# Kernel tuning notes

Hardware: AMD Instinct MI355X
Metric: run time of the kernel (lower is better)

## Reference

```python
import jax, jax.numpy as jnp
import numpy as np

N = 100000   # nodes
E = 1600000  # edges
G = 512      # graphs
IN_F = 128
HID = 64
EPS = 1e-5


def setup_inputs() -> dict:
    key = jax.random.key(0)
    ks = jax.random.split(key, 16)
    x = jax.random.normal(ks[0], (N, IN_F), dtype=jnp.float32)
    edge_index = jax.random.randint(ks[1], (2, E), 0, N, dtype=jnp.int64)
    batch = jnp.sort(jax.random.randint(ks[2], (N,), 0, G, dtype=jnp.int64))
    s = 0.05
    return {
        'x': x, 'edge_index': edge_index, 'batch': batch,
        'W1': jax.random.normal(ks[3], (IN_F, HID), jnp.float32) * s,
        'b1': jax.random.normal(ks[4], (HID,), jnp.float32) * s,
        'g1': jax.random.uniform(ks[5], (HID,), jnp.float32),
        'be1': jax.random.normal(ks[6], (HID,), jnp.float32) * s,
        'rm1': jnp.zeros((HID,), jnp.float32),
        'rv1': jnp.ones((HID,), jnp.float32),
        'W2': jax.random.normal(ks[7], (HID, HID), jnp.float32) * s,
        'b2': jax.random.normal(ks[8], (HID,), jnp.float32) * s,
        'g2': jax.random.uniform(ks[9], (HID,), jnp.float32),
        'be2': jax.random.normal(ks[10], (HID,), jnp.float32) * s,
        'rm2': jnp.zeros((HID,), jnp.float32),
        'rv2': jnp.ones((HID,), jnp.float32),
        'Wh1': jax.random.normal(ks[11], (2 * HID, HID), jnp.float32) * s,
        'bh1': jax.random.normal(ks[12], (HID,), jnp.float32) * s,
        'Wh2': jax.random.normal(ks[13], (HID, HID // 2), jnp.float32) * s,
        'bh2': jnp.zeros((HID // 2,), jnp.float32),
        'Wh3': jax.random.normal(ks[14], (HID // 2, 1), jnp.float32) * s,
        'bh3': jnp.zeros((1,), jnp.float32),
    }


def _gcn(h, W, b, src, dst):
    # GCNConv with added self-loops and symmetric D^{-1/2} A D^{-1/2} normalization
    hw = h @ W                                   # [N, HID]
    deg = jnp.ones((N,), hw.dtype).at[dst].add(1.0)  # in-degree + self-loop
    dinv = jax.lax.rsqrt(deg)
    norm = dinv[src] * dinv[dst]                 # [E]
    agg = jax.ops.segment_sum(hw[src] * norm[:, None], dst, num_segments=N)
    return agg + hw * (dinv * dinv)[:, None] + b  # self-loop term + bias


def _bn(x, g, b, rm, rv):
    return (x - rm) * jax.lax.rsqrt(rv + EPS) * g + b


def reference(x, edge_index, batch, W1, b1, g1, be1, rm1, rv1,
              W2, b2, g2, be2, rm2, rv2, Wh1, bh1, Wh2, bh2, Wh3, bh3):
    src, dst = edge_index[0], edge_index[1]
    # layer 0 (no residual: dim change 128 -> 64)
    h = jax.nn.relu(_bn(_gcn(x, W1, b1, src, dst), g1, be1, rm1, rv1))
    # layer 1 with residual
    h = h + jax.nn.relu(_bn(_gcn(h, W2, b2, src, dst), g2, be2, rm2, rv2))
    # global mean + max pooling per graph
    ones = jnp.ones((N,), h.dtype)
    cnt = jnp.maximum(jax.ops.segment_sum(ones, batch, num_segments=G), 1.0)
    h_mean = jax.ops.segment_sum(h, batch, num_segments=G) / cnt[:, None]
    h_max = jax.ops.segment_max(h, batch, num_segments=G)
    hg = jnp.concatenate([h_mean, h_max], axis=-1)   # [G, 2*HID]
    # MLP head (dropout disabled in eval)
    z = jax.nn.relu(hg @ Wh1 + bh1)
    z = jax.nn.relu(z @ Wh2 + bh2)
    out = z @ Wh3 + bh3
    return jax.nn.sigmoid(out).squeeze(-1)           # [G]
```

## Files before the change

### kernel.cpp

```cpp
#include <hip/hip_runtime.h>
#include <math.h>

#define NN 100000
#define EE 1600000
#define GG 512
#define INF_ 128
#define HID 64
#define EPS 1e-5f

#define NBUK 391
#define P1_TILES 98
#define P1_PAD 104
#define GB_B 25
#define GEMM1_B 1563

typedef unsigned int uint32;
typedef __attribute__((ext_vector_type(8))) short bf16x8;
typedef __attribute__((ext_vector_type(4))) float f32x4;
typedef __attribute__((ext_vector_type(2))) float f32x2;

static __device__ inline uint32 f2bf(float f) {
    uint32 u = __float_as_uint(f);
    return (u + 0x7FFFu + ((u >> 16) & 1u)) >> 16;
}


template <int K, bool SCALE>
__device__ __forceinline__ void gemm_body(const float* __restrict__ X,
        const float* __restrict__ W, const float* __restrict__ dinv,
        uint32* __restrict__ outb, int nrows, int bx,
        unsigned short* __restrict__ Al, unsigned short* __restrict__ Bl) {
    constexpr int KP = K + 8;
    int tid = threadIdx.x;
    for (int i = tid; i < 64 * (K / 2); i += 256) {
        int n = i & 63, kp = i >> 6;
        uint32 lo = f2bf(W[(size_t)(2 * kp) * 64 + n]);
        uint32 hi = f2bf(W[(size_t)(2 * kp + 1) * 64 + n]);
        *(uint32*)&Bl[n * KP + kp * 2] = lo | (hi << 16);
    }
    int r0 = bx * 64;
    const float* Xb = X + (size_t)r0 * K;
    int limit = (nrows - r0) * K;
    for (int f = tid * 4; f < 64 * K; f += 1024) {
        float4 v = {0.f, 0.f, 0.f, 0.f};
        if (f + 3 < limit) v = *(const float4*)&Xb[f];
        int row = f / K, kpos = f % K;
        ushort4 pk;
        pk.x = (unsigned short)f2bf(v.x);
        pk.y = (unsigned short)f2bf(v.y);
        pk.z = (unsigned short)f2bf(v.z);
        pk.w = (unsigned short)f2bf(v.w);
        *(ushort4*)&Al[row * KP + kpos] = pk;
    }
    __syncthreads();
    int lane = tid & 63, wv = tid >> 6;
    int m = lane & 15, quad = lane >> 4;
    f32x4 acc0 = {0.f, 0.f, 0.f, 0.f}, acc1 = acc0, acc2 = acc0, acc3 = acc0;
    int arow = wv * 16 + m;
#pragma unroll
    for (int k0 = 0; k0 < K; k0 += 32) {
        int koff = k0 + quad * 8;
        bf16x8 a = *(const bf16x8*)&Al[arow * KP + koff];
        bf16x8 b0 = *(const bf16x8*)&Bl[(0 * 16 + m) * KP + koff];
        bf16x8 b1 = *(const bf16x8*)&Bl[(1 * 16 + m) * KP + koff];
        bf16x8 b2 = *(const bf16x8*)&Bl[(2 * 16 + m) * KP + koff];
        bf16x8 b3 = *(const bf16x8*)&Bl[(3 * 16 + m) * KP + koff];
        acc0 = __builtin_amdgcn_mfma_f32_16x16x32_bf16(a, b0, acc0, 0, 0, 0);
        acc1 = __builtin_amdgcn_mfma_f32_16x16x32_bf16(a, b1, acc1, 0, 0, 0);
        acc2 = __builtin_amdgcn_mfma_f32_16x16x32_bf16(a, b2, acc2, 0, 0, 0);
        acc3 = __builtin_amdgcn_mfma_f32_16x16x32_bf16(a, b3, acc3, 0, 0, 0);
    }
    float dv[4];
#pragma unroll
    for (int reg = 0; reg < 4; ++reg) {
        int row = r0 + wv * 16 + quad * 4 + reg;
        if (SCALE) dv[reg] = (row < nrows) ? dinv[row] : 0.f;
        else       dv[reg] = 1.f;
    }
    const float* accs[4] = {(const float*)&acc0, (const float*)&acc1,
                            (const float*)&acc2, (const float*)&acc3};
#pragma unroll
    for (int nt = 0; nt < 4; ++nt) {
#pragma unroll
        for (int reg = 0; reg < 4; ++reg) {
            float val = accs[nt][reg] * dv[reg];
            float v1 = __shfl_down(val, 1);
            float v2 = __shfl_down(val, 2);
            float v3 = __shfl_down(val, 3);
            int row = r0 + wv * 16 + quad * 4 + reg;
            if (((m & 3) == 0) && row < nrows) {
                int u = __builtin_amdgcn_cvt_pk_fp8_f32(val, v1, 0, false);
                u = __builtin_amdgcn_cvt_pk_fp8_f32(v2, v3, u, true);
                outb[(size_t)row * 16 + nt * 4 + (m >> 2)] = (uint32)u;
            }
        }
    }
}

__global__ __launch_bounds__(256) void k_mega(const int* __restrict__ ei,
        int* __restrict__ hblk, const int* __restrict__ bat, int* __restrict__ gb,
        const float* __restrict__ x, const float* __restrict__ W1,
        uint32* __restrict__ hwb,
        const float* b1, const float* g1, const float* be1,
        const float* rm1, const float* rv1,
        const float* b2, const float* g2, const float* be2,
        const float* rm2, const float* rv2, float* sc) {
    __shared__ alignas(16) char smem[64 * (INF_ + 8) * 2 * 2];
    int b = blockIdx.x, t = threadIdx.x;
    if (b < P1_TILES) {
        int* h = (int*)smem;
        for (int i = t; i < NBUK; i += 256) h[i] = 0;
        __syncthreads();
        const int4* dst4 = (const int4*)(ei + EE);
        int base4 = b * 4096;
        for (int j = 0; j < 16; ++j) {
            int i4 = base4 + j * 256 + t;
            if (i4 < EE / 4) {
                int4 d = dst4[i4];
                atomicAdd(&h[d.x >> 8], 1);
                atomicAdd(&h[d.y >> 8], 1);
                atomicAdd(&h[d.z >> 8], 1);
                atomicAdd(&h[d.w >> 8], 1);
            }
        }
        __syncthreads();
        for (int i = t; i < NBUK; i += 256) hblk[i * P1_PAD + b] = h[i];
    } else if (b < P1_TILES + GB_B) {
        int gid = (b - P1_TILES) * 256 + t;
        for (int i = gid; i < NN; i += GB_B * 256) {
            int bi = bat[i];
            if (i == 0) {
                for (int g = 0; g <= bi; ++g) gb[g] = 0;
            } else {
                int bp = bat[i - 1];
                for (int g = bp + 1; g <= bi; ++g) gb[g] = i;
            }
            if (i == NN - 1)
                for (int g = bi + 1; g <= GG; ++g) gb[g] = NN;
        }
    } else if (b < P1_TILES + GB_B + 1) {
        if (t < 64) {
            int l = t;
            float s1 = g1[l] * rsqrtf(rv1[l] + EPS);
            sc[l]       = s1;
            sc[64 + l]  = (b1[l] - rm1[l]) * s1 + be1[l];
            float s2 = g2[l] * rsqrtf(rv2[l] + EPS);
            sc[128 + l] = s2;
            sc[192 + l] = (b2[l] - rm2[l]) * s2 + be2[l];
        } else if (t < 80) {
            hwb[(size_t)NN * 16 + (t - 64)] = 0u;
        }
        for (int i = t; i < NBUK * (P1_PAD - P1_TILES); i += 256) {
            int k = i / (P1_PAD - P1_TILES);
            int bb = P1_TILES + i % (P1_PAD - P1_TILES);
            hblk[k * P1_PAD + bb] = 0;
        }
    } else {
        int bx = b - P1_TILES - GB_B - 1;
        unsigned short* Al = (unsigned short*)smem;
        unsigned short* Bl = (unsigned short*)(smem + 64 * (INF_ + 8) * 2);
        gemm_body<INF_, false>(x, W1, nullptr, hwb, NN, bx, Al, Bl);
    }
}

__global__ __launch_bounds__(512) void k_p1b(const int* __restrict__ ei,
                                             const int* __restrict__ hblk,
                                             uint32* __restrict__ pairs,
                                             int* __restrict__ bbase,
                                             int* __restrict__ offs) {
    __shared__ int h[NBUK];
    __shared__ int wsum[8];
    int b = blockIdx.x, t = threadIdx.x;
    int part = 0, c = 0;
    if (t < NBUK) {
        const int4* row = (const int4*)(hblk + t * P1_PAD);
#pragma unroll
        for (int q = 0; q < P1_PAD / 4; ++q) {
            int4 v = row[q];
            c += v.x + v.y + v.z + v.w;
            part += ((4 * q + 0 < b) ? v.x : 0) + ((4 * q + 1 < b) ? v.y : 0)
                  + ((4 * q + 2 < b) ? v.z : 0) + ((4 * q + 3 < b) ? v.w : 0);
        }
    }
    int lane = t & 63, w = t >> 6;
    int v = c;
    for (int d = 1; d < 64; d <<= 1) { int n = __shfl_up(v, d); if (lane >= d) v += n; }
    if (lane == 63) wsum[w] = v;
    __syncthreads();
    int pre = 0;
    for (int q = 0; q < w; ++q) pre += wsum[q];
    int excl = pre + v - c;
    if (t < NBUK) h[t] = excl + part;
    if (b == 0) {
        if (t <= NBUK) bbase[t] = excl;
        if (t == 0) offs[NN] = EE;
    }
    __syncthreads();
    const int4* src4 = (const int4*)ei;
    const int4* dst4 = (const int4*)(ei + EE);
    int base4 = b * 4096;
    for (int j = 0; j < 8; ++j) {
        int i4 = base4 + j * 512 + t;
        if (i4 < EE / 4) {
            int4 d = dst4[i4];
            int4 s = src4[i4];
            int p0 = atomicAdd(&h[d.x >> 8], 1);
            pairs[p0] = ((uint32)s.x << 8) | (uint32)(d.x & 255);
            int p1 = atomicAdd(&h[d.y >> 8], 1);
            pairs[p1] = ((uint32)s.y << 8) | (uint32)(d.y & 255);
            int p2 = atomicAdd(&h[d.z >> 8], 1);
            pairs[p2] = ((uint32)s.z << 8) | (uint32)(d.z & 255);
            int p3 = atomicAdd(&h[d.w >> 8], 1);
            pairs[p3] = ((uint32)s.w << 8) | (uint32)(d.w & 255);
        }
    }
}

__global__ __launch_bounds__(256) void k_p2(const uint32* __restrict__ pairs,
                                            const int* __restrict__ bbase,
                                            int* __restrict__ offs, float* __restrict__ dinv,
                                            int* __restrict__ col) {
    int b = blockIdx.x, t = threadIdx.x;
    int nbase = b << 8;
    int ebase = bbase[b], eend = bbase[b + 1];
    int m = eend - ebase;
    __shared__ int cnt[256];
    __shared__ int wsum[4];
    cnt[t] = 0;
    __syncthreads();
    for (int i = t; i < m; i += 256)
        atomicAdd(&cnt[pairs[ebase + i] & 255u], 1);
    __syncthreads();
    int c = cnt[t];
    int lane = t & 63, w = t >> 6;
    int v = c;
    for (int d = 1; d < 64; d <<= 1) { int n = __shfl_up(v, d); if (lane >= d) v += n; }
    if (lane == 63) wsum[w] = v;
    __syncthreads();
    int pre = 0;
    for (int q = 0; q < w; ++q) pre += wsum[q];
    int excl = pre + v - c;
    int node = nbase + t;
    if (node < NN) {
        offs[node] = ebase + excl;
        dinv[node] = rsqrtf(1.f + (float)c);
    }
    __syncthreads();
    cnt[t] = excl;
    __syncthreads();
    for (int i = t; i < m; i += 256) {
        uint32 u = pairs[ebase + i];
        int loc = atomicAdd(&cnt[u & 255u], 1);
        col[ebase + loc] = (int)(u >> 8);
    }
}

__global__ void k_gcn_gather_w(const uint32* __restrict__ hwb, const int* __restrict__ col,
                               const int* __restrict__ offs,
                               const float* __restrict__ dinv, const float* __restrict__ scale,
                               const float* __restrict__ shift,
                               float* __restrict__ out) {
    int node = blockIdx.x * 4 + (threadIdx.x >> 6);
    if (node >= NN) return;
    int lane = threadIdx.x & 63;
    int quarter = lane >> 4;
    int fl = lane & 15;
    int e0 = offs[node], e1 = offs[node + 1];
    float di = dinv[node];
    uint32 uself = hwb[(size_t)node * 16 + fl];
    float a0 = 0.f, a1 = 0.f, a2 = 0.f, a3 = 0.f;
    float b0 = 0.f, b1 = 0.f, b2 = 0.f, b3 = 0.f;
    for (int base = e0; base < e1; base += 64) {
        int m = e1 - base; if (m > 64) m = 64;
        int srcv = NN; float wv = 0.f;
        if (lane < m) { srcv = col[base + lane]; wv = dinv[srcv]; }
        for (int j = 0; j < m; j += 16) {
            int   s0 = __shfl(srcv, j + quarter);
            int   s1 = __shfl(srcv, j + 4 + quarter);
            int   s2 = __shfl(srcv, j + 8 + quarter);
            int   s3 = __shfl(srcv, j + 12 + quarter);
            float w0 = __shfl(wv, j + quarter);
            float w1 = __shfl(wv, j + 4 + quarter);
            float w2 = __shfl(wv, j + 8 + quarter);
            float w3 = __shfl(wv, j + 12 + quarter);
            uint32 u0 = hwb[(size_t)s0 * 16 + fl];
            uint32 u1 = hwb[(size_t)s1 * 16 + fl];
            uint32 u2 = hwb[(size_t)s2 * 16 + fl];
            uint32 u3 = hwb[(size_t)s3 * 16 + fl];
            f32x2 l0 = __builtin_amdgcn_cvt_pk_f32_fp8((int)u0, false);
            f32x2 h0 = __builtin_amdgcn_cvt_pk_f32_fp8((int)u0, true);
            f32x2 l1 = __builtin_amdgcn_cvt_pk_f32_fp8((int)u1, false);
            f32x2 h1 = __builtin_amdgcn_cvt_pk_f32_fp8((int)u1, true);
            f32x2 l2 = __builtin_amdgcn_cvt_pk_f32_fp8((int)u2, false);
            f32x2 h2 = __builtin_amdgcn_cvt_pk_f32_fp8((int)u2, true);
            f32x2 l3 = __builtin_amdgcn_cvt_pk_f32_fp8((int)u3, false);
            f32x2 h3 = __builtin_amdgcn_cvt_pk_f32_fp8((int)u3, true);
            a0 = fmaf(l0[0], w0, a0); a1 = fmaf(l0[1], w0, a1);
            a2 = fmaf(h0[0], w0, a2); a3 = fmaf(h0[1], w0, a3);
            b0 = fmaf(l1[0], w1, b0); b1 = fmaf(l1[1], w1, b1);
            b2 = fmaf(h1[0], w1, b2); b3 = fmaf(h1[1], w1, b3);
            a0 = fmaf(l2[0], w2, a0); a1 = fmaf(l2[1], w2, a1);
            a2 = fmaf(h2[0], w2, a2); a3 = fmaf(h2[1], w2, a3);
            b0 = fmaf(l3[0], w3, b0); b1 = fmaf(l3[1], w3, b1);
            b2 = fmaf(h3[0], w3, b2); b3 = fmaf(h3[1], w3, b3);
        }
    }
    a0 += b0; a1 += b1; a2 += b2; a3 += b3;
    a0 += __shfl_xor(a0, 16); a0 += __shfl_xor(a0, 32);
    a1 += __shfl_xor(a1, 16); a1 += __shfl_xor(a1, 32);
    a2 += __shfl_xor(a2, 16); a2 += __shfl_xor(a2, 32);
    a3 += __shfl_xor(a3, 16); a3 += __shfl_xor(a3, 32);
    if (quarter == 0) {
        f32x2 slo = __builtin_amdgcn_cvt_pk_f32_fp8((int)uself, false);
        f32x2 shi = __builtin_amdgcn_cvt_pk_f32_fp8((int)uself, true);
        float dii = di * di;
        float4 sc4 = *(const float4*)&scale[4 * fl];
        float4 sh4 = *(const float4*)&shift[4 * fl];
        float v0 = fmaf(a0 * di + slo[0] * dii, sc4.x, sh4.x);
        float v1 = fmaf(a1 * di + slo[1] * dii, sc4.y, sh4.y);
        float v2 = fmaf(a2 * di + shi[0] * dii, sc4.z, sh4.z);
        float v3 = fmaf(a3 * di + shi[1] * dii, sc4.w, sh4.w);
        float4 o;
        o.x = fmaxf(v0, 0.f); o.y = fmaxf(v1, 0.f);
        o.z = fmaxf(v2, 0.f); o.w = fmaxf(v3, 0.f);
        *(float4*)&out[(size_t)node * 64 + 4 * fl] = o;
    }
}

__global__ void k_gcn_gather(const uint32* __restrict__ hwb, const int* __restrict__ col,
                             const int* __restrict__ offs,
                             const float* __restrict__ dinv, const float* __restrict__ scale,
                             const float* __restrict__ shift, const float* __restrict__ resid,
                             float* __restrict__ out) {
    int node = blockIdx.x * 4 + (threadIdx.x >> 6);
    if (node >= NN) return;
    int lane = threadIdx.x & 63;
    int quarter = lane >> 4;
    int fl = lane & 15;
    int e0 = offs[node], e1 = offs[node + 1];
    float di = dinv[node];
    uint32 uself = hwb[(size_t)node * 16 + fl];
    float a0 = 0.f, a1 = 0.f, a2 = 0.f, a3 = 0.f;
    float b0 = 0.f, b1 = 0.f, b2 = 0.f, b3 = 0.f;
    for (int base = e0; base < e1; base += 64) {
        int m = e1 - base; if (m > 64) m = 64;
        int srcv = NN;
        if (lane < m) srcv = col[base + lane];
        for (int j = 0; j < m; j += 16) {
            int s0 = __shfl(srcv, j + quarter);
            int s1 = __shfl(srcv, j + 4 + quarter);
            int s2 = __shfl(srcv, j + 8 + quarter);
            int s3 = __shfl(srcv, j + 12 + quarter);
            uint32 u0 = hwb[(size_t)s0 * 16 + fl];
            uint32 u1 = hwb[(size_t)s1 * 16 + fl];
            uint32 u2 = hwb[(size_t)s2 * 16 + fl];
            uint32 u3 = hwb[(size_t)s3 * 16 + fl];
            f32x2 l0 = __builtin_amdgcn_cvt_pk_f32_fp8((int)u0, false);
            f32x2 h0 = __builtin_amdgcn_cvt_pk_f32_fp8((int)u0, true);
            f32x2 l1 = __builtin_amdgcn_cvt_pk_f32_fp8((int)u1, false);
            f32x2 h1 = __builtin_amdgcn_cvt_pk_f32_fp8((int)u1, true);
            f32x2 l2 = __builtin_amdgcn_cvt_pk_f32_fp8((int)u2, false);
            f32x2 h2 = __builtin_amdgcn_cvt_pk_f32_fp8((int)u2, true);
            f32x2 l3 = __builtin_amdgcn_cvt_pk_f32_fp8((int)u3, false);
            f32x2 h3 = __builtin_amdgcn_cvt_pk_f32_fp8((int)u3, true);
            a0 += l0[0]; a1 += l0[1]; a2 += h0[0]; a3 += h0[1];
            b0 += l1[0]; b1 += l1[1]; b2 += h1[0]; b3 += h1[1];
            a0 += l2[0]; a1 += l2[1]; a2 += h2[0]; a3 += h2[1];
            b0 += l3[0]; b1 += l3[1]; b2 += h3[0]; b3 += h3[1];
        }
    }
    a0 += b0; a1 += b1; a2 += b2; a3 += b3;
    a0 += __shfl_xor(a0, 16); a0 += __shfl_xor(a0, 32);
    a1 += __shfl_xor(a1, 16); a1 += __shfl_xor(a1, 32);
    a2 += __shfl_xor(a2, 16); a2 += __shfl_xor(a2, 32);
    a3 += __shfl_xor(a3, 16); a3 += __shfl_xor(a3, 32);
    if (quarter == 0) {
        f32x2 slo = __builtin_amdgcn_cvt_pk_f32_fp8((int)uself, false);
        f32x2 shi = __builtin_amdgcn_cvt_pk_f32_fp8((int)uself, true);
        float4 sc4 = *(const float4*)&scale[4 * fl];
        float4 sh4 = *(const float4*)&shift[4 * fl];
        float v0 = fmaf((a0 + slo[0]) * di, sc4.x, sh4.x);
        float v1 = fmaf((a1 + slo[1]) * di, sc4.y, sh4.y);
        float v2 = fmaf((a2 + shi[0]) * di, sc4.z, sh4.z);
        float v3 = fmaf((a3 + shi[1]) * di, sc4.w, sh4.w);
        float4 rv = *(const float4*)&resid[(size_t)node * 64 + 4 * fl];
        float4 o;
        o.x = fmaxf(v0, 0.f) + rv.x;
        o.y = fmaxf(v1, 0.f) + rv.y;
        o.z = fmaxf(v2, 0.f) + rv.z;
        o.w = fmaxf(v3, 0.f) + rv.w;
        *(float4*)&out[(size_t)node * 64 + 4 * fl] = o;
    }
}

__global__ void k_poolhead(const float* __restrict__ h, const int* __restrict__ gb,
                           const float* __restrict__ Wh1, const float* __restrict__ bh1,
                           const float* __restrict__ Wh2, const float* __restrict__ bh2,
                           const float* __restrict__ Wh3, const float* __restrict__ bh3,
                           float* __restrict__ out) {
    int g = blockIdx.x, t = threadIdx.x;
    int lo = gb[g], hi = gb[g + 1];
    float s0 = 0.f, s1 = 0.f, s2 = 0.f, s3 = 0.f;
    float s4 = 0.f, s5 = 0.f, s6 = 0.f, s7 = 0.f;
    float m0 = 0.f, m1 = 0.f, m2 = 0.f, m3 = 0.f;
    float m4 = 0.f, m5 = 0.f, m6 = 0.f, m7 = 0.f;
    int i = lo;
    for (; i + 8 <= hi; i += 8) {
        float v0 = h[(size_t)(i + 0) * 64 + t];
        float v1 = h[(size_t)(i + 1) * 64 + t];
        float v2 = h[(size_t)(i + 2) * 64 + t];
        float v3 = h[(size_t)(i + 3) * 64 + t];
        float v4 = h[(size_t)(i + 4) * 64 + t];
        float v5 = h[(size_t)(i + 5) * 64 + t];
        float v6 = h[(size_t)(i + 6) * 64 + t];
        float v7 = h[(size_t)(i + 7) * 64 + t];
        s0 += v0; m0 = fmaxf(m0, v0);
        s1 += v1; m1 = fmaxf(m1, v1);
        s2 += v2; m2 = fmaxf(m2, v2);
        s3 += v3; m3 = fmaxf(m3, v3);
        s4 += v4; m4 = fmaxf(m4, v4);
        s5 += v5; m5 = fmaxf(m5, v5);
        s6 += v6; m6 = fmaxf(m6, v6);
        s7 += v7; m7 = fmaxf(m7, v7);
    }
    for (; i < hi; ++i) {
        float v = h[(size_t)i * 64 + t];
        s0 += v; m0 = fmaxf(m0, v);
    }
    float sum = ((s0 + s1) + (s2 + s3)) + ((s4 + s5) + (s6 + s7));
    float mx = fmaxf(fmaxf(fmaxf(m0, m1), fmaxf(m2, m3)),
                     fmaxf(fmaxf(m4, m5), fmaxf(m6, m7)));
    float c = fmaxf((float)(hi - lo), 1.f);
    __shared__ float hg[128];
    __shared__ float z1[64];
    __shared__ float z2[32];
    hg[t]      = sum / c;
    hg[64 + t] = mx;
    __syncthreads();
    float acc = bh1[t];
#pragma unroll 8
    for (int k = 0; k < 128; ++k) acc = fmaf(hg[k], Wh1[k * 64 + t], acc);
    z1[t] = fmaxf(acc, 0.f);
    __syncthreads();
    if (t < 32) {
        float a2 = bh2[t];
#pragma unroll 8
        for (int k = 0; k < 64; ++k) a2 = fmaf(z1[k], Wh2[k * 32 + t], a2);
        z2[t] = fmaxf(a2, 0.f);
    }
    __syncthreads();
    if (t == 0) {
        float a3 = bh3[0];
        for (int k = 0; k < 32; ++k) a3 = fmaf(z2[k], Wh3[k], a3);
        out[g] = 1.f / (1.f + expf(-a3));
    }
}

__global__ __launch_bounds__(256) void k_gemm2(const float* __restrict__ X,
                                               const float* __restrict__ W,
                                               const float* __restrict__ dinv,
                                               uint32* __restrict__ outb) {
    __shared__ alignas(16) unsigned short Al[64 * (HID + 8)];
    __shared__ alignas(16) unsigned short Bl[64 * (HID + 8)];
    gemm_body<HID, true>(X, W, dinv, outb, NN, blockIdx.x, Al, Bl);
}


static inline size_t alignup(size_t x) { return (x + 255) & ~(size_t)255; }

extern "C" void kernel_launch(void* const* d_in, const int* in_sizes, int n_in,
                              void* d_out, int out_size, void* d_ws, size_t ws_size,
                              hipStream_t stream) {
    const float* x   = (const float*)d_in[0];
    const int*   ei  = (const int*)d_in[1];
    const int*   bat = (const int*)d_in[2];
    const float* W1  = (const float*)d_in[3];
    const float* b1  = (const float*)d_in[4];
    const float* g1  = (const float*)d_in[5];
    const float* be1 = (const float*)d_in[6];
    const float* rm1 = (const float*)d_in[7];
    const float* rv1 = (const float*)d_in[8];
    const float* W2  = (const float*)d_in[9];
    const float* b2  = (const float*)d_in[10];
    const float* g2  = (const float*)d_in[11];
    const float* be2 = (const float*)d_in[12];
    const float* rm2 = (const float*)d_in[13];
    const float* rv2 = (const float*)d_in[14];
    const float* Wh1 = (const float*)d_in[15];
    const float* bh1 = (const float*)d_in[16];
    const float* Wh2 = (const float*)d_in[17];
    const float* bh2 = (const float*)d_in[18];
    const float* Wh3 = (const float*)d_in[19];
    const float* bh3 = (const float*)d_in[20];
    float* out = (float*)d_out;

    char* ws = (char*)d_ws;
    size_t o = 0;
    int*   hblk   = (int*)(ws + o);  o = alignup(o + (size_t)NBUK * P1_PAD * 4);
    int*   bbase  = (int*)(ws + o);  o = alignup(o + (NBUK + 1) * 4);
    int*   offs   = (int*)(ws + o);  o = alignup(o + (NN + 1) * 4);
    uint32* pairs = (uint32*)(ws + o); o = alignup(o + (size_t)EE * 4);
    int*   col    = (int*)(ws + o);  o = alignup(o + (size_t)EE * 4);
    float* dinv   = (float*)(ws + o); o = alignup(o + (size_t)NN * 4);
    float* scb    = (float*)(ws + o); o = alignup(o + 4 * 64 * 4);
    int*   gb     = (int*)(ws + o);  o = alignup(o + (GG + 1) * 4);
    uint32* hwb   = (uint32*)(ws + o); o = alignup(o + (size_t)(NN + 1) * 16 * 4);
    float* h      = (float*)(ws + o); o = alignup(o + (size_t)NN * 64 * 4);
    (void)ws_size; (void)n_in; (void)in_sizes; (void)out_size;

    k_mega<<<P1_TILES + GB_B + 1 + GEMM1_B, 256, 0, stream>>>(
        ei, hblk, bat, gb, x, W1, hwb,
        b1, g1, be1, rm1, rv1, b2, g2, be2, rm2, rv2, scb);
    k_p1b<<<P1_TILES, 512, 0, stream>>>(ei, hblk, pairs, bbase, offs);
    k_p2<<<NBUK, 256, 0, stream>>>(pairs, bbase, offs, dinv, col);

    k_gcn_gather_w<<<(NN + 3) / 4, 256, 0, stream>>>(hwb, col, offs, dinv,
                                                     scb, scb + 64, h);
    k_gemm2<<<GEMM1_B, 256, 0, stream>>>(h, W2, dinv, hwb);
    k_gcn_gather<<<(NN + 3) / 4, 256, 0, stream>>>(hwb, col, offs, dinv,
                                                   scb + 128, scb + 192, h, h);
    k_poolhead<<<GG, 64, 0, stream>>>(h, gb, Wh1, bh1, Wh2, bh2, Wh3, bh3, out);
}
```

Before: 284.8 us.

## Store layer-1 activations as bf16 and process two nodes per wave in gathers

Result: faster. 270.9 us (median of 2 runs) (-4.9%).

```diff
diff --git a/kernel.cpp b/kernel.cpp
--- a/kernel.cpp
+++ b/kernel.cpp
@@ -23,6 +23,8 @@
     uint32 u = __float_as_uint(f);
     return (u + 0x7FFFu + ((u >> 16) & 1u)) >> 16;
 }
+static __device__ inline float bf_lo(uint32 u) { return __uint_as_float(u << 16); }
+static __device__ inline float bf_hi(uint32 u) { return __uint_as_float(u & 0xFFFF0000u); }
 
 
 template <int K, bool SCALE>
@@ -259,137 +261,247 @@
                                const int* __restrict__ offs,
                                const float* __restrict__ dinv, const float* __restrict__ scale,
                                const float* __restrict__ shift,
-                               float* __restrict__ out) {
-    int node = blockIdx.x * 4 + (threadIdx.x >> 6);
-    if (node >= NN) return;
+                               uint32* __restrict__ out) {
+    int nodeA = blockIdx.x * 8 + (threadIdx.x >> 6) * 2;
+    if (nodeA >= NN) return;
+    int nodeB = nodeA + 1;
+    int hasB = nodeB < NN;
     int lane = threadIdx.x & 63;
     int quarter = lane >> 4;
     int fl = lane & 15;
-    int e0 = offs[node], e1 = offs[node + 1];
-    float di = dinv[node];
-    uint32 uself = hwb[(size_t)node * 16 + fl];
-    float a0 = 0.f, a1 = 0.f, a2 = 0.f, a3 = 0.f;
-    float b0 = 0.f, b1 = 0.f, b2 = 0.f, b3 = 0.f;
-    for (int base = e0; base < e1; base += 64) {
-        int m = e1 - base; if (m > 64) m = 64;
-        int srcv = NN; float wv = 0.f;
-        if (lane < m) { srcv = col[base + lane]; wv = dinv[srcv]; }
-        for (int j = 0; j < m; j += 16) {
-            int   s0 = __shfl(srcv, j + quarter);
-            int   s1 = __shfl(srcv, j + 4 + quarter);
-            int   s2 = __shfl(srcv, j + 8 + quarter);
-            int   s3 = __shfl(srcv, j + 12 + quarter);
-            float w0 = __shfl(wv, j + quarter);
-            float w1 = __shfl(wv, j + 4 + quarter);
-            float w2 = __shfl(wv, j + 8 + quarter);
-            float w3 = __shfl(wv, j + 12 + quarter);
-            uint32 u0 = hwb[(size_t)s0 * 16 + fl];
-            uint32 u1 = hwb[(size_t)s1 * 16 + fl];
-            uint32 u2 = hwb[(size_t)s2 * 16 + fl];
-            uint32 u3 = hwb[(size_t)s3 * 16 + fl];
-            f32x2 l0 = __builtin_amdgcn_cvt_pk_f32_fp8((int)u0, false);
-            f32x2 h0 = __builtin_amdgcn_cvt_pk_f32_fp8((int)u0, true);
-            f32x2 l1 = __builtin_amdgcn_cvt_pk_f32_fp8((int)u1, false);
-            f32x2 h1 = __builtin_amdgcn_cvt_pk_f32_fp8((int)u1, true);
-            f32x2 l2 = __builtin_amdgcn_cvt_pk_f32_fp8((int)u2, false);
-            f32x2 h2 = __builtin_amdgcn_cvt_pk_f32_fp8((int)u2, true);
-            f32x2 l3 = __builtin_amdgcn_cvt_pk_f32_fp8((int)u3, false);
-            f32x2 h3 = __builtin_amdgcn_cvt_pk_f32_fp8((int)u3, true);
-            a0 = fmaf(l0[0], w0, a0); a1 = fmaf(l0[1], w0, a1);
-            a2 = fmaf(h0[0], w0, a2); a3 = fmaf(h0[1], w0, a3);
-            b0 = fmaf(l1[0], w1, b0); b1 = fmaf(l1[1], w1, b1);
-            b2 = fmaf(h1[0], w1, b2); b3 = fmaf(h1[1], w1, b3);
-            a0 = fmaf(l2[0], w2, a0); a1 = fmaf(l2[1], w2, a1);
-            a2 = fmaf(h2[0], w2, a2); a3 = fmaf(h2[1], w2, a3);
-            b0 = fmaf(l3[0], w3, b0); b1 = fmaf(l3[1], w3, b1);
-            b2 = fmaf(h3[0], w3, b2); b3 = fmaf(h3[1], w3, b3);
-        }
-    }
-    a0 += b0; a1 += b1; a2 += b2; a3 += b3;
-    a0 += __shfl_xor(a0, 16); a0 += __shfl_xor(a0, 32);
-    a1 += __shfl_xor(a1, 16); a1 += __shfl_xor(a1, 32);
-    a2 += __shfl_xor(a2, 16); a2 += __shfl_xor(a2, 32);
-    a3 += __shfl_xor(a3, 16); a3 += __shfl_xor(a3, 32);
+    int eA0 = offs[nodeA], eA1 = offs[nodeA + 1];
+    int eB1 = hasB ? offs[nodeB + 1] : eA1;
+    int eB0 = eA1;
+    float diA = dinv[nodeA];
+    float diB = hasB ? dinv[nodeB] : 0.f;
+    uint32 uselfA = hwb[(size_t)nodeA * 16 + fl];
+    uint32 uselfB = hwb[(size_t)(hasB ? nodeB : NN) * 16 + fl];
+    float aA0 = 0.f, aA1 = 0.f, aA2 = 0.f, aA3 = 0.f;
+    float aB0 = 0.f, aB1 = 0.f, aB2 = 0.f, aB3 = 0.f;
+    int baseA = eA0, baseB = eB0;
+    while (baseA < eA1 || baseB < eB1) {
+        int mA = eA1 - baseA; mA = mA < 0 ? 0 : (mA > 64 ? 64 : mA);
+        int mB = eB1 - baseB; mB = mB < 0 ? 0 : (mB > 64 ? 64 : mB);
+        int sA = NN; float wA = 0.f;
+        if (lane < mA) { sA = col[baseA + lane]; wA = dinv[sA]; }
+        int sB = NN; float wB = 0.f;
+        if (lane < mB) { sB = col[baseB + lane]; wB = dinv[sB]; }
+        int mm = mA > mB ? mA : mB;
+        for (int j = 0; j < mm; j += 16) {
+            int   sa0 = __shfl(sA, j + quarter);
+            int   sa1 = __shfl(sA, j + 4 + quarter);
+            int   sa2 = __shfl(sA, j + 8 + quarter);
+            int   sa3 = __shfl(sA, j + 12 + quarter);
+            int   sb0 = __shfl(sB, j + quarter);
+            int   sb1 = __shfl(sB, j + 4 + quarter);
+            int   sb2 = __shfl(sB, j + 8 + quarter);
+            int   sb3 = __shfl(sB, j + 12 + quarter);
+            float wa0 = __shfl(wA, j + quarter);
+            float wa1 = __shfl(wA, j + 4 + quarter);
+            float wa2 = __shfl(wA, j + 8 + quarter);
+            float wa3 = __shfl(wA, j + 12 + quarter);
+            float wb0 = __shfl(wB, j + quarter);
+            float wb1 = __shfl(wB, j + 4 + quarter);
+            float wb2 = __shfl(wB, j + 8 + quarter);
+            float wb3 = __shfl(wB, j + 12 + quarter);
+            uint32 ua0 = hwb[(size_t)sa0 * 16 + fl];
+            uint32 ua1 = hwb[(size_t)sa1 * 16 + fl];
+            uint32 ua2 = hwb[(size_t)sa2 * 16 + fl];
+            uint32 ua3 = hwb[(size_t)sa3 * 16 + fl];
+            uint32 ub0 = hwb[(size_t)sb0 * 16 + fl];
+            uint32 ub1 = hwb[(size_t)sb1 * 16 + fl];
+            uint32 ub2 = hwb[(size_t)sb2 * 16 + fl];
+            uint32 ub3 = hwb[(size_t)sb3 * 16 + fl];
+            f32x2 la0 = __builtin_amdgcn_cvt_pk_f32_fp8((int)ua0, false);
+            f32x2 ha0 = __builtin_amdgcn_cvt_pk_f32_fp8((int)ua0, true);
+            f32x2 la1 = __builtin_amdgcn_cvt_pk_f32_fp8((int)ua1, false);
+            f32x2 ha1 = __builtin_amdgcn_cvt_pk_f32_fp8((int)ua1, true);
+            f32x2 la2 = __builtin_amdgcn_cvt_pk_f32_fp8((int)ua2, false);
+            f32x2 ha2 = __builtin_amdgcn_cvt_pk_f32_fp8((int)ua2, true);
+            f32x2 la3 = __builtin_amdgcn_cvt_pk_f32_fp8((int)ua3, false);
+            f32x2 ha3 = __builtin_amdgcn_cvt_pk_f32_fp8((int)ua3, true);
+            f32x2 lb0 = __builtin_amdgcn_cvt_pk_f32_fp8((int)ub0, false);
+            f32x2 hb0 = __builtin_amdgcn_cvt_pk_f32_fp8((int)ub0, true);
+            f32x2 lb1 = __builtin_amdgcn_cvt_pk_f32_fp8((int)ub1, false);
+            f32x2 hb1 = __builtin_amdgcn_cvt_pk_f32_fp8((int)ub1, true);
+            f32x2 lb2 = __builtin_amdgcn_cvt_pk_f32_fp8((int)ub2, false);
+            f32x2 hb2 = __builtin_amdgcn_cvt_pk_f32_fp8((int)ub2, true);
+            f32x2 lb3 = __builtin_amdgcn_cvt_pk_f32_fp8((int)ub3, false);
+            f32x2 hb3 = __builtin_amdgcn_cvt_pk_f32_fp8((int)ub3, true);
+            aA0 = fmaf(la0[0], wa0, aA0); aA1 = fmaf(la0[1], wa0, aA1);
+            aA2 = fmaf(ha0[0], wa0, aA2); aA3 = fmaf(ha0[1], wa0, aA3);
+            aB0 = fmaf(lb0[0], wb0, aB0); aB1 = fmaf(lb0[1], wb0, aB1);
+            aB2 = fmaf(hb0[0], wb0, aB2); aB3 = fmaf(hb0[1], wb0, aB3);
+            aA0 = fmaf(la1[0], wa1, aA0); aA1 = fmaf(la1[1], wa1, aA1);
+            aA2 = fmaf(ha1[0], wa1, aA2); aA3 = fmaf(ha1[1], wa1, aA3);
+            aB0 = fmaf(lb1[0], wb1, aB0); aB1 = fmaf(lb1[1], wb1, aB1);
+            aB2 = fmaf(hb1[0], wb1, aB2); aB3 = fmaf(hb1[1], wb1, aB3);
+            aA0 = fmaf(la2[0], wa2, aA0); aA1 = fmaf(la2[1], wa2, aA1);
+            aA2 = fmaf(ha2[0], wa2, aA2); aA3 = fmaf(ha2[1], wa2, aA3);
+            aB0 = fmaf(lb2[0], wb2, aB0); aB1 = fmaf(lb2[1], wb2, aB1);
+            aB2 = fmaf(hb2[0], wb2, aB2); aB3 = fmaf(hb2[1], wb2, aB3);
+            aA0 = fmaf(la3[0], wa3, aA0); aA1 = fmaf(la3[1], wa3, aA1);
+            aA2 = fmaf(ha3[0], wa3, aA2); aA3 = fmaf(ha3[1], wa3, aA3);
+            aB0 = fmaf(lb3[0], wb3, aB0); aB1 = fmaf(lb3[1], wb3, aB1);
+            aB2 = fmaf(hb3[0], wb3, aB2); aB3 = fmaf(hb3[1], wb3, aB3);
+        }
+        baseA += 64; baseB += 64;
+    }
+    aA0 += __shfl_xor(aA0, 16); aA0 += __shfl_xor(aA0, 32);
+    aA1 += __shfl_xor(aA1, 16); aA1 += __shfl_xor(aA1, 32);
+    aA2 += __shfl_xor(aA2, 16); aA2 += __shfl_xor(aA2, 32);
+    aA3 += __shfl_xor(aA3, 16); aA3 += __shfl_xor(aA3, 32);
+    aB0 += __shfl_xor(aB0, 16); aB0 += __shfl_xor(aB0, 32);
+    aB1 += __shfl_xor(aB1, 16); aB1 += __shfl_xor(aB1, 32);
+    aB2 += __shfl_xor(aB2, 16); aB2 += __shfl_xor(aB2, 32);
+    aB3 += __shfl_xor(aB3, 16); aB3 += __shfl_xor(aB3, 32);
     if (quarter == 0) {
-        f32x2 slo = __builtin_amdgcn_cvt_pk_f32_fp8((int)uself, false);
-        f32x2 shi = __builtin_amdgcn_cvt_pk_f32_fp8((int)uself, true);
-        float dii = di * di;
         float4 sc4 = *(const float4*)&scale[4 * fl];
         float4 sh4 = *(const float4*)&shift[4 * fl];
-        float v0 = fmaf(a0 * di + slo[0] * dii, sc4.x, sh4.x);
-        float v1 = fmaf(a1 * di + slo[1] * dii, sc4.y, sh4.y);
-        float v2 = fmaf(a2 * di + shi[0] * dii, sc4.z, sh4.z);
-        float v3 = fmaf(a3 * di + shi[1] * dii, sc4.w, sh4.w);
-        float4 o;
-        o.x = fmaxf(v0, 0.f); o.y = fmaxf(v1, 0.f);
-        o.z = fmaxf(v2, 0.f); o.w = fmaxf(v3, 0.f);
-        *(float4*)&out[(size_t)node * 64 + 4 * fl] = o;
+        f32x2 sloA = __builtin_amdgcn_cvt_pk_f32_fp8((int)uselfA, false);
+        f32x2 shiA = __builtin_amdgcn_cvt_pk_f32_fp8((int)uselfA, true);
+        float diiA = diA * diA;
+        float v0 = fmaf(aA0 * diA + sloA[0] * diiA, sc4.x, sh4.x);
+        float v1 = fmaf(aA1 * diA + sloA[1] * diiA, sc4.y, sh4.y);
+        float v2 = fmaf(aA2 * diA + shiA[0] * diiA, sc4.z, sh4.z);
+        float v3 = fmaf(aA3 * diA + shiA[1] * diiA, sc4.w, sh4.w);
+        v0 = fmaxf(v0, 0.f); v1 = fmaxf(v1, 0.f);
+        v2 = fmaxf(v2, 0.f); v3 = fmaxf(v3, 0.f);
+        uint2 oA;
+        oA.x = f2bf(v0) | (f2bf(v1) << 16);
+        oA.y = f2bf(v2) | (f2bf(v3) << 16);
+        *(uint2*)&out[(size_t)nodeA * 32 + 2 * fl] = oA;
+        if (hasB) {
+            f32x2 sloB = __builtin_amdgcn_cvt_pk_f32_fp8((int)uselfB, false);
+            f32x2 shiB = __builtin_amdgcn_cvt_pk_f32_fp8((int)uselfB, true);
+            float diiB = diB * diB;
+            float w0 = fmaf(aB0 * diB + sloB[0] * diiB, sc4.x, sh4.x);
+            float w1 = fmaf(aB1 * diB + sloB[1] * diiB, sc4.y, sh4.y);
+            float w2 = fmaf(aB2 * diB + shiB[0] * diiB, sc4.z, sh4.z);
+            float w3 = fmaf(aB3 * diB + shiB[1] * diiB, sc4.w, sh4.w);
+            w0 = fmaxf(w0, 0.f); w1 = fmaxf(w1, 0.f);
+            w2 = fmaxf(w2, 0.f); w3 = fmaxf(w3, 0.f);
+            uint2 oB;
+            oB.x = f2bf(w0) | (f2bf(w1) << 16);
+            oB.y = f2bf(w2) | (f2bf(w3) << 16);
+            *(uint2*)&out[(size_t)nodeB * 32 + 2 * fl] = oB;
+        }
     }
 }
 
 __global__ void k_gcn_gather(const uint32* __restrict__ hwb, const int* __restrict__ col,
                              const int* __restrict__ offs,
                              const float* __restrict__ dinv, const float* __restrict__ scale,
-                             const float* __restrict__ shift, const float* __restrict__ resid,
+                             const float* __restrict__ shift, const uint32* __restrict__ resid,
                              float* __restrict__ out) {
-    int node = blockIdx.x * 4 + (threadIdx.x >> 6);
-    if (node >= NN) return;
+    int nodeA = blockIdx.x * 8 + (threadIdx.x >> 6) * 2;
+    if (nodeA >= NN) return;
+    int nodeB = nodeA + 1;
+    int hasB = nodeB < NN;
     int lane = threadIdx.x & 63;
     int quarter = lane >> 4;
     int fl = lane & 15;
-    int e0 = offs[node], e1 = offs[node + 1];
-    float di = dinv[node];
-    uint32 uself = hwb[(size_t)node * 16 + fl];
-    float a0 = 0.f, a1 = 0.f, a2 = 0.f, a3 = 0.f;
-    float b0 = 0.f, b1 = 0.f, b2 = 0.f, b3 = 0.f;
-    for (int base = e0; base < e1; base += 64) {
-        int m = e1 - base; if (m > 64) m = 64;
-        int srcv = NN;
-        if (lane < m) srcv = col[base + lane];
-        for (int j = 0; j < m; j += 16) {
-            int s0 = __shfl(srcv, j + quarter);
-            int s1 = __shfl(srcv, j + 4 + quarter);
-            int s2 = __shfl(srcv, j + 8 + quarter);
-            int s3 = __shfl(srcv, j + 12 + quarter);
-            uint32 u0 = hwb[(size_t)s0 * 16 + fl];
-            uint32 u1 = hwb[(size_t)s1 * 16 + fl];
-            uint32 u2 = hwb[(size_t)s2 * 16 + fl];
-            uint32 u3 = hwb[(size_t)s3 * 16 + fl];
-            f32x2 l0 = __builtin_amdgcn_cvt_pk_f32_fp8((int)u0, false);
-            f32x2 h0 = __builtin_amdgcn_cvt_pk_f32_fp8((int)u0, true);
-            f32x2 l1 = __builtin_amdgcn_cvt_pk_f32_fp8((int)u1, false);
-            f32x2 h1 = __builtin_amdgcn_cvt_pk_f32_fp8((int)u1, true);
-            f32x2 l2 = __builtin_amdgcn_cvt_pk_f32_fp8((int)u2, false);
-            f32x2 h2 = __builtin_amdgcn_cvt_pk_f32_fp8((int)u2, true);
-            f32x2 l3 = __builtin_amdgcn_cvt_pk_f32_fp8((int)u3, false);
-            f32x2 h3 = __builtin_amdgcn_cvt_pk_f32_fp8((int)u3, true);
-            a0 += l0[0]; a1 += l0[1]; a2 += h0[0]; a3 += h0[1];
-            b0 += l1[0]; b1 += l1[1]; b2 += h1[0]; b3 += h1[1];
-            a0 += l2[0]; a1 += l2[1]; a2 += h2[0]; a3 += h2[1];
-            b0 += l3[0]; b1 += l3[1]; b2 += h3[0]; b3 += h3[1];
-        }
-    }
-    a0 += b0; a1 += b1; a2 += b2; a3 += b3;
-    a0 += __shfl_xor(a0, 16); a0 += __shfl_xor(a0, 32);
-    a1 += __shfl_xor(a1, 16); a1 += __shfl_xor(a1, 32);
-    a2 += __shfl_xor(a2, 16); a2 += __shfl_xor(a2, 32);
-    a3 += __shfl_xor(a3, 16); a3 += __shfl_xor(a3, 32);
+    int eA0 = offs[nodeA], eA1 = offs[nodeA + 1];
+    int eB1 = hasB ? offs[nodeB + 1] : eA1;
+    int eB0 = eA1;
+    float diA = dinv[nodeA];
+    float diB = hasB ? dinv[nodeB] : 0.f;
+    uint32 uselfA = hwb[(size_t)nodeA * 16 + fl];
+    uint32 uselfB = hwb[(size_t)(hasB ? nodeB : NN) * 16 + fl];
+    float aA0 = 0.f, aA1 = 0.f, aA2 = 0.f, aA3 = 0.f;
+    float aB0 = 0.f, aB1 = 0.f, aB2 = 0.f, aB3 = 0.f;
+    int baseA = eA0, baseB = eB0;
+    while (baseA < eA1 || baseB < eB1) {
+        int mA = eA1 - baseA; mA = mA < 0 ? 0 : (mA > 64 ? 64 : mA);
+        int mB = eB1 - baseB; mB = mB < 0 ? 0 : (mB > 64 ? 64 : mB);
+        int sA = NN;
+        if (lane < mA) sA = col[baseA + lane];
+        int sB = NN;
+        if (lane < mB) sB = col[baseB + lane];
+        int mm = mA > mB ? mA : mB;
+        for (int j = 0; j < mm; j += 16) {
+            int sa0 = __shfl(sA, j + quarter);
+            int sa1 = __shfl(sA, j + 4 + quarter);
+            int sa2 = __shfl(sA, j + 8 + quarter);
+            int sa3 = __shfl(sA, j + 12 + quarter);
+            int sb0 = __shfl(sB, j + quarter);
+            int sb1 = __shfl(sB, j + 4 + quarter);
+            int sb2 = __shfl(sB, j + 8 + quarter);
+            int sb3 = __shfl(sB, j + 12 + quarter);
+            uint32 ua0 = hwb[(size_t)sa0 * 16 + fl];
+            uint32 ua1 = hwb[(size_t)sa1 * 16 + fl];
+            uint32 ua2 = hwb[(size_t)sa2 * 16 + fl];
+            uint32 ua3 = hwb[(size_t)sa3 * 16 + fl];
+            uint32 ub0 = hwb[(size_t)sb0 * 16 + fl];
+            uint32 ub1 = hwb[(size_t)sb1 * 16 + fl];
+            uint32 ub2 = hwb[(size_t)sb2 * 16 + fl];
+            uint32 ub3 = hwb[(size_t)sb3 * 16 + fl];
+            f32x2 la0 = __builtin_amdgcn_cvt_pk_f32_fp8((int)ua0, false);
+            f32x2 ha0 = __builtin_amdgcn_cvt_pk_f32_fp8((int)ua0, true);
+            f32x2 la1 = __builtin_amdgcn_cvt_pk_f32_fp8((int)ua1, false);
+            f32x2 ha1 = __builtin_amdgcn_cvt_pk_f32_fp8((int)ua1, true);
+            f32x2 la2 = __builtin_amdgcn_cvt_pk_f32_fp8((int)ua2, false);
+            f32x2 ha2 = __builtin_amdgcn_cvt_pk_f32_fp8((int)ua2, true);
+            f32x2 la3 = __builtin_amdgcn_cvt_pk_f32_fp8((int)ua3, false);
+            f32x2 ha3 = __builtin_amdgcn_cvt_pk_f32_fp8((int)ua3, true);
+            f32x2 lb0 = __builtin_amdgcn_cvt_pk_f32_fp8((int)ub0, false);
+            f32x2 hb0 = __builtin_amdgcn_cvt_pk_f32_fp8((int)ub0, true);
+            f32x2 lb1 = __builtin_amdgcn_cvt_pk_f32_fp8((int)ub1, false);
+            f32x2 hb1 = __builtin_amdgcn_cvt_pk_f32_fp8((int)ub1, true);
+            f32x2 lb2 = __builtin_amdgcn_cvt_pk_f32_fp8((int)ub2, false);
+            f32x2 hb2 = __builtin_amdgcn_cvt_pk_f32_fp8((int)ub2, true);
+            f32x2 lb3 = __builtin_amdgcn_cvt_pk_f32_fp8((int)ub3, false);
+            f32x2 hb3 = __builtin_amdgcn_cvt_pk_f32_fp8((int)ub3, true);
+            aA0 += la0[0]; aA1 += la0[1]; aA2 += ha0[0]; aA3 += ha0[1];
+            aB0 += lb0[0]; aB1 += lb0[1]; aB2 += hb0[0]; aB3 += hb0[1];
+            aA0 += la1[0]; aA1 += la1[1]; aA2 += ha1[0]; aA3 += ha1[1];
+            aB0 += lb1[0]; aB1 += lb1[1]; aB2 += hb1[0]; aB3 += hb1[1];
+            aA0 += la2[0]; aA1 += la2[1]; aA2 += ha2[0]; aA3 += ha2[1];
+            aB0 += lb2[0]; aB1 += lb2[1]; aB2 += hb2[0]; aB3 += hb2[1];
+            aA0 += la3[0]; aA1 += la3[1]; aA2 += ha3[0]; aA3 += ha3[1];
+            aB0 += lb3[0]; aB1 += lb3[1]; aB2 += hb3[0]; aB3 += hb3[1];
+        }
+        baseA += 64; baseB += 64;
+    }
+    aA0 += __shfl_xor(aA0, 16); aA0 += __shfl_xor(aA0, 32);
+    aA1 += __shfl_xor(aA1, 16); aA1 += __shfl_xor(aA1, 32);
+    aA2 += __shfl_xor(aA2, 16); aA2 += __shfl_xor(aA2, 32);
+    aA3 += __shfl_xor(aA3, 16); aA3 += __shfl_xor(aA3, 32);
+    aB0 += __shfl_xor(aB0, 16); aB0 += __shfl_xor(aB0, 32);
+    aB1 += __shfl_xor(aB1, 16); aB1 += __shfl_xor(aB1, 32);
+    aB2 += __shfl_xor(aB2, 16); aB2 += __shfl_xor(aB2, 32);
+    aB3 += __shfl_xor(aB3, 16); aB3 += __shfl_xor(aB3, 32);
     if (quarter == 0) {
-        f32x2 slo = __builtin_amdgcn_cvt_pk_f32_fp8((int)uself, false);
-        f32x2 shi = __builtin_amdgcn_cvt_pk_f32_fp8((int)uself, true);
         float4 sc4 = *(const float4*)&scale[4 * fl];
         float4 sh4 = *(const float4*)&shift[4 * fl];
-        float v0 = fmaf((a0 + slo[0]) * di, sc4.x, sh4.x);
-        float v1 = fmaf((a1 + slo[1]) * di, sc4.y, sh4.y);
-        float v2 = fmaf((a2 + shi[0]) * di, sc4.z, sh4.z);
-        float v3 = fmaf((a3 + shi[1]) * di, sc4.w, sh4.w);
-        float4 rv = *(const float4*)&resid[(size_t)node * 64 + 4 * fl];
-        float4 o;
-        o.x = fmaxf(v0, 0.f) + rv.x;
-        o.y = fmaxf(v1, 0.f) + rv.y;
-        o.z = fmaxf(v2, 0.f) + rv.z;
-        o.w = fmaxf(v3, 0.f) + rv.w;
-        *(float4*)&out[(size_t)node * 64 + 4 * fl] = o;
+        f32x2 sloA = __builtin_amdgcn_cvt_pk_f32_fp8((int)uselfA, false);
+        f32x2 shiA = __builtin_amdgcn_cvt_pk_f32_fp8((int)uselfA, true);
+        float v0 = fmaf((aA0 + sloA[0]) * diA, sc4.x, sh4.x);
+        float v1 = fmaf((aA1 + sloA[1]) * diA, sc4.y, sh4.y);
+        float v2 = fmaf((aA2 + shiA[0]) * diA, sc4.z, sh4.z);
+        float v3 = fmaf((aA3 + shiA[1]) * diA, sc4.w, sh4.w);
+        uint2 rvA = *(const uint2*)&resid[(size_t)nodeA * 32 + 2 * fl];
+        float4 oA;
+        oA.x = fmaxf(v0, 0.f) + bf_lo(rvA.x);
+        oA.y = fmaxf(v1, 0.f) + bf_hi(rvA.x);
+        oA.z = fmaxf(v2, 0.f) + bf_lo(rvA.y);
+        oA.w = fmaxf(v3, 0.f) + bf_hi(rvA.y);
+        *(float4*)&out[(size_t)nodeA * 64 + 4 * fl] = oA;
+        if (hasB) {
+            f32x2 sloB = __builtin_amdgcn_cvt_pk_f32_fp8((int)uselfB, false);
+            f32x2 shiB = __builtin_amdgcn_cvt_pk_f32_fp8((int)uselfB, true);
+            float w0 = fmaf((aB0 + sloB[0]) * diB, sc4.x, sh4.x);
+            float w1 = fmaf((aB1 + sloB[1]) * diB, sc4.y, sh4.y);
+            float w2 = fmaf((aB2 + shiB[0]) * diB, sc4.z, sh4.z);
+            float w3 = fmaf((aB3 + shiB[1]) * diB, sc4.w, sh4.w);
+            uint2 rvB = *(const uint2*)&resid[(size_t)nodeB * 32 + 2 * fl];
+            float4 oB;
+            oB.x = fmaxf(w0, 0.f) + bf_lo(rvB.x);
+            oB.y = fmaxf(w1, 0.f) + bf_hi(rvB.x);
+            oB.z = fmaxf(w2, 0.f) + bf_lo(rvB.y);
+            oB.w = fmaxf(w3, 0.f) + bf_hi(rvB.y);
+            *(float4*)&out[(size_t)nodeB * 64 + 4 * fl] = oB;
+        }
     }
 }
 
@@ -456,13 +568,71 @@
     }
 }
 
-__global__ __launch_bounds__(256) void k_gemm2(const float* __restrict__ X,
+__global__ __launch_bounds__(256) void k_gemm2(const uint32* __restrict__ Xb16,
                                                const float* __restrict__ W,
                                                const float* __restrict__ dinv,
                                                uint32* __restrict__ outb) {
-    __shared__ alignas(16) unsigned short Al[64 * (HID + 8)];
-    __shared__ alignas(16) unsigned short Bl[64 * (HID + 8)];
-    gemm_body<HID, true>(X, W, dinv, outb, NN, blockIdx.x, Al, Bl);
+    constexpr int K = HID, KP = K + 8;
+    __shared__ alignas(16) unsigned short Al[64 * KP];
+    __shared__ alignas(16) unsigned short Bl[64 * KP];
+    int tid = threadIdx.x;
+    for (int i = tid; i < 64 * (K / 2); i += 256) {
+        int n = i & 63, kp = i >> 6;
+        uint32 lo = f2bf(W[(size_t)(2 * kp) * 64 + n]);
+        uint32 hi = f2bf(W[(size_t)(2 * kp + 1) * 64 + n]);
+        *(uint32*)&Bl[n * KP + kp * 2] = lo | (hi << 16);
+    }
+    int r0 = blockIdx.x * 64;
+    const uint32* Xr = Xb16 + (size_t)r0 * 32;
+    int limit = (NN - r0) * 32;
+    for (int f = tid * 4; f < 64 * 32; f += 1024) {
+        uint4 v = {0u, 0u, 0u, 0u};
+        if (f + 3 < limit) v = *(const uint4*)&Xr[f];
+        int row = f >> 5, kpos = (f & 31) * 2;
+        *(uint4*)&Al[row * KP + kpos] = v;
+    }
+    __syncthreads();
+    int lane = tid & 63, wv = tid >> 6;
+    int m = lane & 15, quad = lane >> 4;
+    f32x4 acc0 = {0.f, 0.f, 0.f, 0.f}, acc1 = acc0, acc2 = acc0, acc3 = acc0;
+    int arow = wv * 16 + m;
+#pragma unroll
+    for (int k0 = 0; k0 < K; k0 += 32) {
+        int koff = k0 + quad * 8;
+        bf16x8 a = *(const bf16x8*)&Al[arow * KP + koff];
+        bf16x8 b0 = *(const bf16x8*)&Bl[(0 * 16 + m) * KP + koff];
+        bf16x8 b1 = *(const bf16x8*)&Bl[(1 * 16 + m) * KP + koff];
+        bf16x8 b2 = *(const bf16x8*)&Bl[(2 * 16 + m) * KP + koff];
+        bf16x8 b3 = *(const bf16x8*)&Bl[(3 * 16 + m) * KP + koff];
+        acc0 = __builtin_amdgcn_mfma_f32_16x16x32_bf16(a, b0, acc0, 0, 0, 0);
+        acc1 = __builtin_amdgcn_mfma_f32_16x16x32_bf16(a, b1, acc1, 0, 0, 0);
+        acc2 = __builtin_amdgcn_mfma_f32_16x16x32_bf16(a, b2, acc2, 0, 0, 0);
+        acc3 = __builtin_amdgcn_mfma_f32_16x16x32_bf16(a, b3, acc3, 0, 0, 0);
+    }
+    float dv[4];
+#pragma unroll
+    for (int reg = 0; reg < 4; ++reg) {
+        int row = r0 + wv * 16 + quad * 4 + reg;
+        dv[reg] = (row < NN) ? dinv[row] : 0.f;
+    }
+    const float* accs[4] = {(const float*)&acc0, (const float*)&acc1,
+                            (const float*)&acc2, (const float*)&acc3};
+#pragma unroll
+    for (int nt = 0; nt < 4; ++nt) {
+#pragma unroll
+        for (int reg = 0; reg < 4; ++reg) {
+            float val = accs[nt][reg] * dv[reg];
+            float v1 = __shfl_down(val, 1);
+            float v2 = __shfl_down(val, 2);
+            float v3 = __shfl_down(val, 3);
+            int row = r0 + wv * 16 + quad * 4 + reg;
+            if (((m & 3) == 0) && row < NN) {
+                int u = __builtin_amdgcn_cvt_pk_fp8_f32(val, v1, 0, false);
+                u = __builtin_amdgcn_cvt_pk_fp8_f32(v2, v3, u, true);
+                outb[(size_t)row * 16 + nt * 4 + (m >> 2)] = (uint32)u;
+            }
+        }
+    }
 }
 
 
@@ -505,6 +675,7 @@
     float* scb    = (float*)(ws + o); o = alignup(o + 4 * 64 * 4);
     int*   gb     = (int*)(ws + o);  o = alignup(o + (GG + 1) * 4);
     uint32* hwb   = (uint32*)(ws + o); o = alignup(o + (size_t)(NN + 1) * 16 * 4);
+    uint32* h1b   = (uint32*)(ws + o); o = alignup(o + (size_t)NN * 32 * 4);
     float* h      = (float*)(ws + o); o = alignup(o + (size_t)NN * 64 * 4);
     (void)ws_size; (void)n_in; (void)in_sizes; (void)out_size;
 
@@ -514,10 +685,10 @@
     k_p1b<<<P1_TILES, 512, 0, stream>>>(ei, hblk, pairs, bbase, offs);
     k_p2<<<NBUK, 256, 0, stream>>>(pairs, bbase, offs, dinv, col);
 
-    k_gcn_gather_w<<<(NN + 3) / 4, 256, 0, stream>>>(hwb, col, offs, dinv,
-                                                     scb, scb + 64, h);
-    k_gemm2<<<GEMM1_B, 256, 0, stream>>>(h, W2, dinv, hwb);
-    k_gcn_gather<<<(NN + 3) / 4, 256, 0, stream>>>(hwb, col, offs, dinv,
-                                                   scb + 128, scb + 192, h, h);
+    k_gcn_gather_w<<<(NN + 7) / 8, 256, 0, stream>>>(hwb, col, offs, dinv,
+                                                     scb, scb + 64, h1b);
+    k_gemm2<<<GEMM1_B, 256, 0, stream>>>(h1b, W2, dinv, hwb);
+    k_gcn_gather<<<(NN + 7) / 8, 256, 0, stream>>>(hwb, col, offs, dinv,
+                                                   scb + 128, scb + 192, h1b, h);
     k_poolhead<<<GG, 64, 0, stream>>>(h, gb, Wh1, bh1, Wh2, bh2, Wh3, bh3, out);
 }
```
